# Kernel tuning notes

Hardware: AMD Instinct MI355X
Metric: run time of the kernel (lower is better)

## Reference

```python
import jax, jax.numpy as jnp
import numpy as np

N_HEADS = 16


def setup_inputs() -> dict:
    key = jax.random.key(0)
    ks = jax.random.split(key, 9)
    B, S, D = 2, 2048, 1024
    sc = 0.02
    return {
        'x': jax.random.normal(ks[0], (B, S, D), jnp.float32),
        'Wq': jax.random.normal(ks[1], (D, D), jnp.float32) * sc,
        'bq': jax.random.normal(ks[2], (D,), jnp.float32) * sc,
        'Wk': jax.random.normal(ks[3], (D, D), jnp.float32) * sc,
        'bk': jax.random.normal(ks[4], (D,), jnp.float32) * sc,
        'Wv': jax.random.normal(ks[5], (D, D), jnp.float32) * sc,
        'bv': jax.random.normal(ks[6], (D,), jnp.float32) * sc,
        'Wo': jax.random.normal(ks[7], (D, D), jnp.float32) * sc,
        'bo': jax.random.normal(ks[8], (D,), jnp.float32) * sc,
    }


def reference(x, Wq, bq, Wk, bk, Wv, bv, Wo, bo):
    # Chunked causal prefill. The chunk-wise mask (q_pos >= kv_pos over the
    # growing KV cache) is mathematically identical to full causal attention,
    # so we compute it as one vectorized masked softmax attention.
    B, S, D = x.shape
    H = N_HEADS
    hd = D // H

    def proj(W, b):
        # torch Linear: y = x @ W.T + b ; then split heads -> [B,H,S,hd]
        y = jnp.einsum('bsd,ed->bse', x, W) + b
        return y.reshape(B, S, H, hd).transpose(0, 2, 1, 3)

    q = proj(Wq, bq)
    k = proj(Wk, bk)
    v = proj(Wv, bv)

    scores = jnp.einsum('bhqd,bhkd->bhqk', q, k) / jnp.sqrt(jnp.asarray(hd, x.dtype))
    causal = jnp.tril(jnp.ones((S, S), dtype=bool))  # [S,S]
    scores = jnp.where(causal[None, None], scores, jnp.asarray(-jnp.inf, scores.dtype))
    attn = jax.nn.softmax(scores, axis=-1)
    ctx = jnp.einsum('bhqk,bhkd->bhqd', attn, v)  # [B,H,S,hd]
    ctx = ctx.transpose(0, 2, 1, 3).reshape(B, S, D)
    out = jnp.einsum('bsd,ed->bse', ctx, Wo) + bo
    return out
```

## Files before the change

### kernel.cpp

```cpp
#include <hip/hip_runtime.h>
#include <cstdint>
#include <math.h>

typedef _Float16 f16;
typedef _Float16 f16x2 __attribute__((ext_vector_type(2)));
typedef _Float16 f16x4 __attribute__((ext_vector_type(4)));
typedef _Float16 f16x8 __attribute__((ext_vector_type(8)));
typedef __fp16   h16x2 __attribute__((ext_vector_type(2)));
typedef float    f32x4 __attribute__((ext_vector_type(4)));

__device__ __forceinline__ f32x4 mfma16(f16x8 a, f16x8 b, f32x4 c) {
  return __builtin_amdgcn_mfma_f32_16x16x32_f16(a, b, c, 0, 0, 0);
}
__device__ __forceinline__ void gl2lds16(const f16* g, f16* l) {
  __builtin_amdgcn_global_load_lds((__attribute__((address_space(1))) void*)(g),
                                   (__attribute__((address_space(3))) void*)(l),
                                   16, 0, 0);
}
__device__ __forceinline__ float fexp2(float x) { return __builtin_amdgcn_exp2f(x); }
__device__ __forceinline__ f16x2 pkrtz(float a, float b) {
  h16x2 r = __builtin_amdgcn_cvt_pkrtz(a, b);
  return __builtin_bit_cast(f16x2, r);
}
__device__ __forceinline__ float dot2acc(f16x2 a, f16x2 b, float c) {
#if __has_builtin(__builtin_amdgcn_fdot2)
  return __builtin_amdgcn_fdot2(__builtin_bit_cast(h16x2, a),
                                __builtin_bit_cast(h16x2, b), c, false);
#else
  return c + (float)a[0] * (float)b[0] + (float)a[1] * (float)b[1];
#endif
}

__global__ __launch_bounds__(256) void cvt_kernel(
    const float* __restrict__ x,  const float* __restrict__ wq, const float* __restrict__ wk,
    const float* __restrict__ wv, const float* __restrict__ wo,
    f16* __restrict__ xh, f16* __restrict__ wqkvh, f16* __restrict__ woh)
{
  const int seg = blockIdx.y;
  const float* src; f16* dst; int n;
  if      (seg == 0) { src = x;  dst = xh;              n = 4194304; }
  else if (seg == 1) { src = wq; dst = wqkvh;           n = 1048576; }
  else if (seg == 2) { src = wk; dst = wqkvh + 1048576; n = 1048576; }
  else if (seg == 3) { src = wv; dst = wqkvh + 2097152; n = 1048576; }
  else               { src = wo; dst = woh;             n = 1048576; }
  const int idx = (int)(blockIdx.x * 256 + threadIdx.x) * 8;
  if (idx >= n) return;
  f32x4 a = *(const f32x4*)(src + idx);
  f32x4 b = *(const f32x4*)(src + idx + 4);
  f16x8 h;
  h[0] = (f16)a[0]; h[1] = (f16)a[1]; h[2] = (f16)a[2]; h[3] = (f16)a[3];
  h[4] = (f16)b[0]; h[5] = (f16)b[1]; h[6] = (f16)b[2]; h[7] = (f16)b[3];
  *(f16x8*)(dst + idx) = h;
}

__global__ __launch_bounds__(256) void gemm_qkv(
    const f16* __restrict__ A, const f16* __restrict__ B,
    const float* __restrict__ bias0, const float* __restrict__ bias1, const float* __restrict__ bias2,
    f16* __restrict__ Qp, f16* __restrict__ Kp, f16* __restrict__ Vp)
{
  constexpr int K = 1024;
  __shared__ __align__(16) f16 As[128 * 32];
  __shared__ __align__(16) f16 Bs[128 * 32];
  const int tid  = threadIdx.x;
  const int wave = tid >> 6, lane = tid & 63;
  const int quad = lane >> 4, col = lane & 15;
  const int tile_m = blockIdx.y * 128, tile_n = blockIdx.x * 128;
  const int mb = (wave >> 1) * 64, nb = (wave & 1) * 64;
  const int srow = lane >> 2, scol = (lane & 3) * 8;
  const f16* gA = A + (size_t)(tile_m + wave * 32 + srow) * K + scol;
  const f16* gB = B + (size_t)(tile_n + wave * 32 + srow) * K + scol;
  f16* lA = As + wave * 1024;
  f16* lB = Bs + wave * 1024;

  f32x4 acc[4][4] = {};
  for (int k0 = 0; k0 < K; k0 += 32) {
    gl2lds16(gA + k0,          lA);
    gl2lds16(gA + 16 * K + k0, lA + 512);
    gl2lds16(gB + k0,          lB);
    gl2lds16(gB + 16 * K + k0, lB + 512);
    __syncthreads();
    f16x8 af[4], bf[4];
    #pragma unroll
    for (int i = 0; i < 4; ++i)
      af[i] = *(const f16x8*)&As[(mb + i * 16 + col) * 32 + quad * 8];
    #pragma unroll
    for (int j = 0; j < 4; ++j)
      bf[j] = *(const f16x8*)&Bs[(nb + j * 16 + col) * 32 + quad * 8];
    #pragma unroll
    for (int i = 0; i < 4; ++i)
      #pragma unroll
      for (int j = 0; j < 4; ++j)
        acc[i][j] = mfma16(af[i], bf[j], acc[i][j]);
    __syncthreads();
  }

  #pragma unroll
  for (int j = 0; j < 4; ++j) {
    const int gn = tile_n + nb + j * 16 + col;
    const int which = gn >> 10;
    const int d = gn & 1023;
    const float* bp = (which == 0) ? bias0 : (which == 1) ? bias1 : bias2;
    f16* dst        = (which == 0) ? Qp    : (which == 1) ? Kp    : Vp;
    const float bvv = bp[d];
    const float qs  = (which == 0) ? 0.18033688f : 1.0f;
    const int h = d >> 6, hi = d & 63;
    #pragma unroll
    for (int i = 0; i < 4; ++i) {
      #pragma unroll
      for (int r = 0; r < 4; ++r) {
        const int gm = tile_m + mb + i * 16 + quad * 4 + r;
        const int bb = gm >> 11, s = gm & 2047;
        dst[(((size_t)bb * 16 + h) * 2048 + s) * 64 + hi] = (f16)((acc[i][j][r] + bvv) * qs);
      }
    }
  }
}

__global__ __launch_bounds__(256) void vtrans_kernel(
    const f16* __restrict__ Vh, f16* __restrict__ Vt)
{
  __shared__ __align__(16) f16 t[64][72];
  const int bh = blockIdx.y;
  const int s0 = blockIdx.x * 64;
  const int tid = threadIdx.x;
  const int sr = tid >> 2, dc = (tid & 3) * 16;
  const size_t ib = ((size_t)bh * 2048 + s0 + sr) * 64 + dc;
  f16x8 v0 = *(const f16x8*)&Vh[ib];
  f16x8 v1 = *(const f16x8*)&Vh[ib + 8];
  *(f16x8*)&t[sr][dc]     = v0;
  *(f16x8*)&t[sr][dc + 8] = v1;
  __syncthreads();
  const int d = tid >> 2, sc = (tid & 3) * 16;
  f16x8 o0, o1;
  #pragma unroll
  for (int j = 0; j < 8; ++j) { o0[j] = t[sc + j][d]; o1[j] = t[sc + 8 + j][d]; }
  const size_t ob = ((size_t)bh * 64 + d) * 2048 + s0 + sc;
  *(f16x8*)&Vt[ob]     = o0;
  *(f16x8*)&Vt[ob + 8] = o1;
}

__global__ __launch_bounds__(128) void attn_kernel(
    const f16* __restrict__ Q, const f16* __restrict__ K, const f16* __restrict__ Vt,
    f16* __restrict__ ctx)
{
  __shared__ __align__(16) f16 Ks[64 * 72];
  __shared__ __align__(16) f16 Vts[64 * 72];
  __shared__ __align__(16) f16 Ps[2][32 * 72];
  __shared__ __align__(16) float abuf[2][32];
  __shared__ __align__(16) float lbuf[2][32];

  const int bh  = blockIdx.y;
  const int tid = threadIdx.x;
  const int wave = tid >> 6, lane = tid & 63;
  const int quad = lane >> 4, col = lane & 15;
  const int b = bh >> 4, h = bh & 15;
  const size_t base = (size_t)bh * 2048 * 64;
  const size_t vtb  = (size_t)bh * 64 * 2048;

  int srow[4], sc8[4];
  #pragma unroll
  for (int i = 0; i < 4; ++i) {
    const int flat = tid + i * 128;
    srow[i] = flat >> 3;
    sc8[i]  = (flat & 7) * 8;
  }

  auto run_tile = [&](int qt) {
    const int q0 = qt * 64;
    const int qa = q0 + wave * 16;
    const int qb = q0 + 32 + wave * 16;
    const f16x8 bqa0 = *(const f16x8*)&Q[base + (size_t)(qa + col) * 64 + quad * 8];
    const f16x8 bqa1 = *(const f16x8*)&Q[base + (size_t)(qa + col) * 64 + 32 + quad * 8];
    const f16x8 bqb0 = *(const f16x8*)&Q[base + (size_t)(qb + col) * 64 + quad * 8];
    const f16x8 bqb1 = *(const f16x8*)&Q[base + (size_t)(qb + col) * 64 + 32 + quad * 8];

    f32x4 cta[4] = {}, ctb[4] = {};
    float ma = -INFINITY, la = 0.f, mb = -INFINITY, lb = 0.f;

    f16x8 kr[4], vr[4];
    auto gload = [&](int t) {
      #pragma unroll
      for (int i = 0; i < 4; ++i) {
        kr[i] = *(const f16x8*)&K[base + (size_t)(t * 64 + srow[i]) * 64 + sc8[i]];
        vr[i] = *(const f16x8*)&Vt[vtb + (size_t)srow[i] * 2048 + t * 64 + sc8[i]];
      }
    };
    gload(0);

    const int nIter = qt + 1;
    for (int t = 0; t < nIter; ++t) {
      __syncthreads();
      #pragma unroll
      for (int i = 0; i < 4; ++i) {
        *(f16x8*)&Ks[srow[i] * 72 + sc8[i]]  = kr[i];
        *(f16x8*)&Vts[srow[i] * 72 + sc8[i]] = vr[i];
      }
      __syncthreads();
      if (t + 1 < nIter) gload(t + 1);

      f32x4 sa[4], sb[4];
      #pragma unroll
      for (int jt = 0; jt < 4; ++jt) {
        const int kro = (jt * 16 + col) * 72;
        const f16x8 ak0 = *(const f16x8*)&Ks[kro + quad * 8];
        const f16x8 ak1 = *(const f16x8*)&Ks[kro + 32 + quad * 8];
        f32x4 za = {}, zb = {};
        za = mfma16(ak0, bqa0, za); sa[jt] = mfma16(ak1, bqa1, za);
        zb = mfma16(ak0, bqb0, zb); sb[jt] = mfma16(ak1, bqb1, zb);
      }

      if (t == qt) {
        #pragma unroll
        for (int jt = 0; jt < 4; ++jt) {
          const int kg = t * 64 + jt * 16 + quad * 4;
          #pragma unroll
          for (int r = 0; r < 4; ++r) {
            if (kg + r > qa + col) sa[jt][r] = -1e30f;
            if (kg + r > qb + col) sb[jt][r] = -1e30f;
          }
        }
      }

      const f16x2 one2 = {(_Float16)1.f, (_Float16)1.f};
      {
        float tm = fmaxf(fmaxf(sa[0][0], sa[0][1]), fmaxf(sa[0][2], sa[0][3]));
        #pragma unroll
        for (int jt = 1; jt < 4; ++jt)
          tm = fmaxf(tm, fmaxf(fmaxf(sa[jt][0], sa[jt][1]), fmaxf(sa[jt][2], sa[jt][3])));
        tm = fmaxf(tm, __shfl_xor(tm, 16));
        tm = fmaxf(tm, __shfl_xor(tm, 32));
        const float mnew = fmaxf(ma, tm);
        const float alpha = fexp2(ma - mnew);
        ma = mnew;
        float rs = 0.f;
        #pragma unroll
        for (int jt = 0; jt < 4; ++jt) {
          const f16x2 a01 = pkrtz(fexp2(sa[jt][0] - mnew), fexp2(sa[jt][1] - mnew));
          const f16x2 a23 = pkrtz(fexp2(sa[jt][2] - mnew), fexp2(sa[jt][3] - mnew));
          rs = dot2acc(a01, one2, rs);
          rs = dot2acc(a23, one2, rs);
          f16x4 pw; pw[0] = a01[0]; pw[1] = a01[1]; pw[2] = a23[0]; pw[3] = a23[1];
          *(f16x4*)&Ps[wave][col * 72 + jt * 16 + quad * 4] = pw;
        }
        rs += __shfl_xor(rs, 16);
        rs += __shfl_xor(rs, 32);
        la = la * alpha + rs;
        if (quad == 0) abuf[wave][col] = alpha;
      }
      {
        float tm = fmaxf(fmaxf(sb[0][0], sb[0][1]), fmaxf(sb[0][2], sb[0][3]));
        #pragma unroll
        for (int jt = 1; jt < 4; ++jt)
          tm = fmaxf(tm, fmaxf(fmaxf(sb[jt][0], sb[jt][1]), fmaxf(sb[jt][2], sb[jt][3])));
        tm = fmaxf(tm, __shfl_xor(tm, 16));
        tm = fmaxf(tm, __shfl_xor(tm, 32));
        const float mnew = fmaxf(mb, tm);
        const float alpha = fexp2(mb - mnew);
        mb = mnew;
        float rs = 0.f;
        #pragma unroll
        for (int jt = 0; jt < 4; ++jt) {
          const f16x2 a01 = pkrtz(fexp2(sb[jt][0] - mnew), fexp2(sb[jt][1] - mnew));
          const f16x2 a23 = pkrtz(fexp2(sb[jt][2] - mnew), fexp2(sb[jt][3] - mnew));
          rs = dot2acc(a01, one2, rs);
          rs = dot2acc(a23, one2, rs);
          f16x4 pw; pw[0] = a01[0]; pw[1] = a01[1]; pw[2] = a23[0]; pw[3] = a23[1];
          *(f16x4*)&Ps[wave][(16 + col) * 72 + jt * 16 + quad * 4] = pw;
        }
        rs += __shfl_xor(rs, 16);
        rs += __shfl_xor(rs, 32);
        lb = lb * alpha + rs;
        if (quad == 0) abuf[wave][16 + col] = alpha;
      }

      __asm__ volatile("s_waitcnt lgkmcnt(0)" ::: "memory");
      const f32x4 ava = *(const f32x4*)&abuf[wave][quad * 4];
      const f32x4 avb = *(const f32x4*)&abuf[wave][16 + quad * 4];
      #pragma unroll
      for (int jd = 0; jd < 4; ++jd) { cta[jd] *= ava; ctb[jd] *= avb; }

      const f16x8 apa0 = *(const f16x8*)&Ps[wave][col * 72 + quad * 8];
      const f16x8 apa1 = *(const f16x8*)&Ps[wave][col * 72 + 32 + quad * 8];
      const f16x8 apb0 = *(const f16x8*)&Ps[wave][(16 + col) * 72 + quad * 8];
      const f16x8 apb1 = *(const f16x8*)&Ps[wave][(16 + col) * 72 + 32 + quad * 8];
      #pragma unroll
      for (int jd = 0; jd < 4; ++jd) {
        const int vro = (jd * 16 + col) * 72;
        const f16x8 bv0 = *(const f16x8*)&Vts[vro + quad * 8];
        const f16x8 bv1 = *(const f16x8*)&Vts[vro + 32 + quad * 8];
        cta[jd] = mfma16(apa1, bv1, mfma16(apa0, bv0, cta[jd]));
        ctb[jd] = mfma16(apb1, bv1, mfma16(apb0, bv0, ctb[jd]));
      }
    }

    if (quad == 0) { lbuf[wave][col] = la; lbuf[wave][16 + col] = lb; }
    __asm__ volatile("s_waitcnt lgkmcnt(0)" ::: "memory");
    const f32x4 lva = *(const f32x4*)&lbuf[wave][quad * 4];
    const f32x4 lvb = *(const f32x4*)&lbuf[wave][16 + quad * 4];
    #pragma unroll
    for (int jd = 0; jd < 4; ++jd) {
      #pragma unroll
      for (int r = 0; r < 4; ++r) {
        const int qga = qa + quad * 4 + r;
        const int qgb = qb + quad * 4 + r;
        const int d = h * 64 + jd * 16 + col;
        ctx[((size_t)b * 2048 + qga) * 1024 + d] = (f16)(cta[jd][r] / lva[r]);
        ctx[((size_t)b * 2048 + qgb) * 1024 + d] = (f16)(ctb[jd][r] / lvb[r]);
      }
    }
  };

  run_tile(blockIdx.x);
  run_tile(31 - blockIdx.x);
}

__global__ __launch_bounds__(256) void gemm_o(
    const f16* __restrict__ A, const f16* __restrict__ B, const float* __restrict__ bias,
    float* __restrict__ Out)
{
  constexpr int K = 1024;
  __shared__ __align__(16) f16 As[128 * 32];
  __shared__ __align__(16) f16 Bs[64 * 32];
  const int tid  = threadIdx.x;
  const int wave = tid >> 6, lane = tid & 63;
  const int quad = lane >> 4, col = lane & 15;
  const int tile_m = blockIdx.y * 128, tile_n = blockIdx.x * 64;
  const int mb = wave * 32;
  const int srow = lane >> 2, scol = (lane & 3) * 8;
  const f16* gA = A + (size_t)(tile_m + wave * 32 + srow) * K + scol;
  const f16* gB = B + (size_t)(tile_n + wave * 16 + srow) * K + scol;
  f16* lA = As + wave * 1024;
  f16* lB = Bs + wave * 512;

  f32x4 acc[2][4] = {};
  for (int k0 = 0; k0 < K; k0 += 32) {
    gl2lds16(gA + k0,          lA);
    gl2lds16(gA + 16 * K + k0, lA + 512);
    gl2lds16(gB + k0,          lB);
    __syncthreads();
    f16x8 af[2], bf[4];
    #pragma unroll
    for (int i = 0; i < 2; ++i)
      af[i] = *(const f16x8*)&As[(mb + i * 16 + col) * 32 + quad * 8];
    #pragma unroll
    for (int j = 0; j < 4; ++j)
      bf[j] = *(const f16x8*)&Bs[(j * 16 + col) * 32 + quad * 8];
    #pragma unroll
    for (int i = 0; i < 2; ++i)
      #pragma unroll
      for (int j = 0; j < 4; ++j)
        acc[i][j] = mfma16(af[i], bf[j], acc[i][j]);
    __syncthreads();
  }

  #pragma unroll
  for (int j = 0; j < 4; ++j) {
    const int gn = tile_n + j * 16 + col;
    const float bvv = bias[gn];
    #pragma unroll
    for (int i = 0; i < 2; ++i) {
      #pragma unroll
      for (int r = 0; r < 4; ++r) {
        const int gm = tile_m + mb + i * 16 + quad * 4 + r;
        Out[(size_t)gm * 1024 + gn] = acc[i][j][r] + bvv;
      }
    }
  }
}

extern "C" void kernel_launch(void* const* d_in, const int* in_sizes, int n_in,
                              void* d_out, int out_size, void* d_ws, size_t ws_size,
                              hipStream_t stream)
{
  const float* x  = (const float*)d_in[0];
  const float* Wq = (const float*)d_in[1];
  const float* bq = (const float*)d_in[2];
  const float* Wk = (const float*)d_in[3];
  const float* bk = (const float*)d_in[4];
  const float* Wv = (const float*)d_in[5];
  const float* bv = (const float*)d_in[6];
  const float* Wo = (const float*)d_in[7];
  const float* bo = (const float*)d_in[8];
  float* out = (float*)d_out;

  f16* ws = (f16*)d_ws;
  const size_t M1 = 1048576;
  f16* xh    = ws;
  f16* wqkvh = ws + 4  * M1;
  f16* woh   = ws + 7  * M1;
  f16* Qh    = ws + 8  * M1;
  f16* Kh    = ws + 12 * M1;
  f16* Vh    = ws + 16 * M1;
  f16* Vth   = ws + 20 * M1;
  f16* ctxh  = ws + 24 * M1;

  cvt_kernel<<<dim3(2048, 5), 256, 0, stream>>>(x, Wq, Wk, Wv, Wo, xh, wqkvh, woh);
  gemm_qkv<<<dim3(24, 32), 256, 0, stream>>>(xh, wqkvh, bq, bk, bv, Qh, Kh, Vh);
  vtrans_kernel<<<dim3(32, 32), 256, 0, stream>>>(Vh, Vth);
  attn_kernel<<<dim3(16, 32), 128, 0, stream>>>(Qh, Kh, Vth, ctxh);
  gemm_o<<<dim3(16, 32), 256, 0, stream>>>(ctxh, woh, bo, out);
}
```

Baseline: 206.0 us.

## Split attention query tile across four waves with one 16-row strip each

The attention block moves from 2 waves each handling two 16-row query strips to 4 waves each handling a single strip, with launch bounds and the block size raised to 256. K/V tile loading is spread over twice as many threads, and the per-wave P, alpha and l buffers are resized. This raises wave-level parallelism and cuts per-thread register pressure. In exchange each K/V tile's LDS reads are amortized over fewer rows per wave, and the block-wide barriers now synchronize more waves.

After: 197.4 us. -4.2%, faster.

```diff
diff --git a/kernel.cpp b/kernel.cpp
--- a/kernel.cpp
+++ b/kernel.cpp
@@ -139,15 +139,15 @@
   *(f16x8*)&Vt[ob + 8] = o1;
 }
 
-__global__ __launch_bounds__(128) void attn_kernel(
+__global__ __launch_bounds__(256) void attn_kernel(
     const f16* __restrict__ Q, const f16* __restrict__ K, const f16* __restrict__ Vt,
     f16* __restrict__ ctx)
 {
   __shared__ __align__(16) f16 Ks[64 * 72];
   __shared__ __align__(16) f16 Vts[64 * 72];
-  __shared__ __align__(16) f16 Ps[2][32 * 72];
-  __shared__ __align__(16) float abuf[2][32];
-  __shared__ __align__(16) float lbuf[2][32];
+  __shared__ __align__(16) f16 Ps[4][16 * 72];
+  __shared__ __align__(16) float abuf[4][16];
+  __shared__ __align__(16) float lbuf[4][16];
 
   const int bh  = blockIdx.y;
   const int tid = threadIdx.x;
@@ -157,10 +157,10 @@
   const size_t base = (size_t)bh * 2048 * 64;
   const size_t vtb  = (size_t)bh * 64 * 2048;
 
-  int srow[4], sc8[4];
+  int srow[2], sc8[2];
   #pragma unroll
-  for (int i = 0; i < 4; ++i) {
-    const int flat = tid + i * 128;
+  for (int i = 0; i < 2; ++i) {
+    const int flat = tid + i * 256;
     srow[i] = flat >> 3;
     sc8[i]  = (flat & 7) * 8;
   }
@@ -168,19 +168,16 @@
   auto run_tile = [&](int qt) {
     const int q0 = qt * 64;
     const int qa = q0 + wave * 16;
-    const int qb = q0 + 32 + wave * 16;
     const f16x8 bqa0 = *(const f16x8*)&Q[base + (size_t)(qa + col) * 64 + quad * 8];
     const f16x8 bqa1 = *(const f16x8*)&Q[base + (size_t)(qa + col) * 64 + 32 + quad * 8];
-    const f16x8 bqb0 = *(const f16x8*)&Q[base + (size_t)(qb + col) * 64 + quad * 8];
-    const f16x8 bqb1 = *(const f16x8*)&Q[base + (size_t)(qb + col) * 64 + 32 + quad * 8];
-
-    f32x4 cta[4] = {}, ctb[4] = {};
-    float ma = -INFINITY, la = 0.f, mb = -INFINITY, lb = 0.f;
-
-    f16x8 kr[4], vr[4];
+
+    f32x4 cta[4] = {};
+    float ma = -INFINITY, la = 0.f;
+
+    f16x8 kr[2], vr[2];
     auto gload = [&](int t) {
       #pragma unroll
-      for (int i = 0; i < 4; ++i) {
+      for (int i = 0; i < 2; ++i) {
         kr[i] = *(const f16x8*)&K[base + (size_t)(t * 64 + srow[i]) * 64 + sc8[i]];
         vr[i] = *(const f16x8*)&Vt[vtb + (size_t)srow[i] * 2048 + t * 64 + sc8[i]];
       }
@@ -191,22 +188,22 @@
     for (int t = 0; t < nIter; ++t) {
       __syncthreads();
       #pragma unroll
-      for (int i = 0; i < 4; ++i) {
+      for (int i = 0; i < 2; ++i) {
         *(f16x8*)&Ks[srow[i] * 72 + sc8[i]]  = kr[i];
         *(f16x8*)&Vts[srow[i] * 72 + sc8[i]] = vr[i];
       }
       __syncthreads();
       if (t + 1 < nIter) gload(t + 1);
 
-      f32x4 sa[4], sb[4];
+      f32x4 sa[4];
       #pragma unroll
       for (int jt = 0; jt < 4; ++jt) {
         const int kro = (jt * 16 + col) * 72;
         const f16x8 ak0 = *(const f16x8*)&Ks[kro + quad * 8];
         const f16x8 ak1 = *(const f16x8*)&Ks[kro + 32 + quad * 8];
-        f32x4 za = {}, zb = {};
-        za = mfma16(ak0, bqa0, za); sa[jt] = mfma16(ak1, bqa1, za);
-        zb = mfma16(ak0, bqb0, zb); sb[jt] = mfma16(ak1, bqb1, zb);
+        f32x4 za = {};
+        za = mfma16(ak0, bqa0, za);
+        sa[jt] = mfma16(ak1, bqa1, za);
       }
 
       if (t == qt) {
@@ -216,7 +213,6 @@
           #pragma unroll
           for (int r = 0; r < 4; ++r) {
             if (kg + r > qa + col) sa[jt][r] = -1e30f;
-            if (kg + r > qb + col) sb[jt][r] = -1e30f;
           }
         }
       }
@@ -247,65 +243,33 @@
         la = la * alpha + rs;
         if (quad == 0) abuf[wave][col] = alpha;
       }
-      {
-        float tm = fmaxf(fmaxf(sb[0][0], sb[0][1]), fmaxf(sb[0][2], sb[0][3]));
-        #pragma unroll
-        for (int jt = 1; jt < 4; ++jt)
-          tm = fmaxf(tm, fmaxf(fmaxf(sb[jt][0], sb[jt][1]), fmaxf(sb[jt][2], sb[jt][3])));
-        tm = fmaxf(tm, __shfl_xor(tm, 16));
-        tm = fmaxf(tm, __shfl_xor(tm, 32));
-        const float mnew = fmaxf(mb, tm);
-        const float alpha = fexp2(mb - mnew);
-        mb = mnew;
-        float rs = 0.f;
-        #pragma unroll
-        for (int jt = 0; jt < 4; ++jt) {
-          const f16x2 a01 = pkrtz(fexp2(sb[jt][0] - mnew), fexp2(sb[jt][1] - mnew));
-          const f16x2 a23 = pkrtz(fexp2(sb[jt][2] - mnew), fexp2(sb[jt][3] - mnew));
-          rs = dot2acc(a01, one2, rs);
-          rs = dot2acc(a23, one2, rs);
-          f16x4 pw; pw[0] = a01[0]; pw[1] = a01[1]; pw[2] = a23[0]; pw[3] = a23[1];
-          *(f16x4*)&Ps[wave][(16 + col) * 72 + jt * 16 + quad * 4] = pw;
-        }
-        rs += __shfl_xor(rs, 16);
-        rs += __shfl_xor(rs, 32);
-        lb = lb * alpha + rs;
-        if (quad == 0) abuf[wave][16 + col] = alpha;
-      }
 
       __asm__ volatile("s_waitcnt lgkmcnt(0)" ::: "memory");
       const f32x4 ava = *(const f32x4*)&abuf[wave][quad * 4];
-      const f32x4 avb = *(const f32x4*)&abuf[wave][16 + quad * 4];
-      #pragma unroll
-      for (int jd = 0; jd < 4; ++jd) { cta[jd] *= ava; ctb[jd] *= avb; }
+      #pragma unroll
+      for (int jd = 0; jd < 4; ++jd) cta[jd] *= ava;
 
       const f16x8 apa0 = *(const f16x8*)&Ps[wave][col * 72 + quad * 8];
       const f16x8 apa1 = *(const f16x8*)&Ps[wave][col * 72 + 32 + quad * 8];
-      const f16x8 apb0 = *(const f16x8*)&Ps[wave][(16 + col) * 72 + quad * 8];
-      const f16x8 apb1 = *(const f16x8*)&Ps[wave][(16 + col) * 72 + 32 + quad * 8];
       #pragma unroll
       for (int jd = 0; jd < 4; ++jd) {
         const int vro = (jd * 16 + col) * 72;
         const f16x8 bv0 = *(const f16x8*)&Vts[vro + quad * 8];
         const f16x8 bv1 = *(const f16x8*)&Vts[vro + 32 + quad * 8];
         cta[jd] = mfma16(apa1, bv1, mfma16(apa0, bv0, cta[jd]));
-        ctb[jd] = mfma16(apb1, bv1, mfma16(apb0, bv0, ctb[jd]));
       }
     }
 
-    if (quad == 0) { lbuf[wave][col] = la; lbuf[wave][16 + col] = lb; }
+    if (quad == 0) lbuf[wave][col] = la;
     __asm__ volatile("s_waitcnt lgkmcnt(0)" ::: "memory");
     const f32x4 lva = *(const f32x4*)&lbuf[wave][quad * 4];
-    const f32x4 lvb = *(const f32x4*)&lbuf[wave][16 + quad * 4];
     #pragma unroll
     for (int jd = 0; jd < 4; ++jd) {
       #pragma unroll
       for (int r = 0; r < 4; ++r) {
         const int qga = qa + quad * 4 + r;
-        const int qgb = qb + quad * 4 + r;
         const int d = h * 64 + jd * 16 + col;
         ctx[((size_t)b * 2048 + qga) * 1024 + d] = (f16)(cta[jd][r] / lva[r]);
-        ctx[((size_t)b * 2048 + qgb) * 1024 + d] = (f16)(ctb[jd][r] / lvb[r]);
       }
     }
   };
@@ -397,6 +361,6 @@
   cvt_kernel<<<dim3(2048, 5), 256, 0, stream>>>(x, Wq, Wk, Wv, Wo, xh, wqkvh, woh);
   gemm_qkv<<<dim3(24, 32), 256, 0, stream>>>(xh, wqkvh, bq, bk, bv, Qh, Kh, Vh);
   vtrans_kernel<<<dim3(32, 32), 256, 0, stream>>>(Vh, Vth);
-  attn_kernel<<<dim3(16, 32), 128, 0, stream>>>(Qh, Kh, Vth, ctxh);
+  attn_kernel<<<dim3(16, 32), 256, 0, stream>>>(Qh, Kh, Vth, ctxh);
   gemm_o<<<dim3(16, 32), 256, 0, stream>>>(ctxh, woh, bo, out);
 }
```
